# Optimization experiments

Measured on AMD Instinct MI355X. Metric: run time of the kernel, lower is better.

The kernel has to match this reference:

```python
import jax, jax.numpy as jnp
import numpy as np
from jax import lax

SIGMA = 5
RADIUS = int(4 * SIGMA + 0.5)  # 20 -> kernel size 41, pad_size = 41//2 = 20 = RADIUS
D_AP = 2.27
D_DV = 2.27


def _gauss_d1_kernel():
    # gaussian_kernel1d(sigma, order=1, radius): q(x) = -x/sigma^2, kernel = q(x)*phi(x)
    x = np.arange(-RADIUS, RADIUS + 1).astype(np.float64)
    phi = np.exp(-0.5 / SIGMA ** 2 * x ** 2)
    phi = phi / phi.sum()
    return ((-x / SIGMA ** 2) * phi).astype(np.float32)

_KERNEL = jnp.asarray(_gauss_d1_kernel())


def _conv1d_valid(x, k):
    # x: [N, L], k: [K] -> [N, L-K+1]; cross-correlation, same as torch F.conv1d
    return lax.conv_general_dilated(x[:, None, :], k[None, None, :], (1,), 'VALID')[:, 0, :]


def diffY(x):
    # circular padding along H, derivative / dDV
    c, h, w = x.shape
    xp = jnp.pad(x, ((0, 0), (RADIUS, RADIUS), (0, 0)), mode='wrap')
    xp = jnp.transpose(xp, (0, 2, 1)).reshape(c * w, h + 2 * RADIUS)
    out = _conv1d_valid(xp, _KERNEL).reshape(c, w, h)
    return jnp.transpose(out, (0, 2, 1)) / D_DV


def diffX(x):
    # reflect padding along W, derivative / dAP
    c, h, w = x.shape
    xp = jnp.pad(x, ((0, 0), (0, 0), (RADIUS, RADIUS)), mode='reflect')
    out = _conv1d_valid(xp.reshape(c * h, w + 2 * RADIUS), _KERNEL).reshape(c, h, w)
    return out / D_AP


def setup_inputs() -> dict:
    key = jax.random.key(0)
    k1, k2, k3, k4, k5 = jax.random.split(key, 5)
    H, W = 1024, 2048
    return {
        'y': jax.random.normal(k1, (5, H, W), dtype=jnp.float32),
        'v': jax.random.normal(k2, (2, H, W), dtype=jnp.float32),
        'gamma_ds': jax.random.normal(k3, (H, W), dtype=jnp.float32),
        'cad_coefs': jax.random.uniform(k4, (3,), dtype=jnp.float32),
        'myo_coefs': jax.random.uniform(k5, (5,), dtype=jnp.float32),
    }


def reference(y, v, gamma_ds, cad_coefs, myo_coefs):
    H, W = y.shape[-2:]
    m4 = y[:4]                                  # [4,H,W] myosin components
    c1 = y[4:]                                  # [1,H,W] cadherin

    d1_m = jnp.stack([diffY(m4), diffX(m4)], axis=-1).reshape(2, 2, H, W, 2)
    m = m4.reshape(2, 2, H, W)
    d1_c = jnp.stack([diffY(c1), diffX(c1)], axis=-1).reshape(H, W, 2)
    c = c1[0]

    d1_v = jnp.stack([diffY(v), diffX(v)], axis=-1)   # [2,H,W,2]: d1_v[i,y,x,j] = d_j v_i
    gv = jnp.einsum('iyxj->ijyx', d1_v)
    gvT = jnp.einsum('jyxi->ijyx', d1_v)
    O = -0.5 * (gv - gvT)                       # vorticity
    E = 0.5 * (gv + gvT)                        # strain rate

    eye = jnp.eye(2, dtype=y.dtype)[:, :, None, None]
    trm_yx = jnp.einsum('kkyx->yx', m)
    deviatoric = m - 0.5 * trm_yx[None, None] * eye

    m_norm = jnp.sqrt(jnp.sum(m * m, axis=(0, 1), keepdims=True))            # [1,1,H,W]
    m_0 = jnp.mean(m_norm, axis=(2, 3), keepdims=True)                       # [1,1,1,1]
    dev_mag = jnp.sqrt(jnp.sum(deviatoric * deviatoric, axis=(0, 1), keepdims=True))
    devE = jnp.einsum('klyx,klyx->yx', deviatoric, E)[None, None]

    E_active = E - jnp.sign(devE) * devE * deviatoric / dev_mag ** 2
    E_active = 0.5 * E_active * dev_mag / m_0
    E_passive = E - E_active

    mE = (jnp.einsum('ikyx,kjyx->ijyx', m, E_passive)
          + jnp.einsum('ikyx,kjyx->ijyx', E_passive, m))

    cad = jax.nn.relu(cad_coefs)
    myo = jax.nn.relu(myo_coefs)

    cdot = (-jnp.einsum('iyx,yxi->yx', v, d1_c)
            - cad[0] * c
            + cad[1] * c * jnp.einsum('iyxi->yx', d1_v)
            + cad[2] * gamma_ds)

    trm = trm_yx[None, None]
    gamma_dv = jnp.array([[1.0, 0.0], [0.0, 0.0]], dtype=y.dtype)[:, :, None, None]

    mdot = (-jnp.einsum('kyx,ijyxk->ijyx', v, d1_m)
            - jnp.einsum('ikyx,kjyx->ijyx', O, m)
            + jnp.einsum('ikyx,kjyx->ijyx', m, O)
            - myo[0] * m
            + myo[1] * mE
            - myo[2] * c[None, None] * mE
            + myo[3] * trm * gamma_dv
            + myo[4] * trm * m)

    return jnp.concatenate([mdot.reshape(4, H, W), cdot[None]], axis=0)
```

## Files before the change

kernel.cpp:

```cpp
#include <hip/hip_runtime.h>
#include <math.h>

#define RAD 20
#define KLEN 41
#define NH 1024
#define NW 2048
#define NHW (NH * NW)

struct KW { float w[KLEN]; };
constexpr double cexp_neg(double u) {
  double term = 1.0, sum = 1.0;
  for (int k = 1; k < 30; ++k) { term *= (-u) / (double)k; sum += term; }
  return sum;
}
constexpr KW make_kw() {
  KW r{};
  double ph[KLEN] = {};
  double s = 0.0;
  for (int i = 0; i < KLEN; ++i) {
    double d = (double)(i - RAD);
    double e = cexp_neg(d * d / 800.0);
    e = e * e; e = e * e; e = e * e; e = e * e;
    ph[i] = e; s += e;
  }
  for (int i = 0; i < KLEN; ++i) {
    double d = (double)(i - RAD);
    r.w[i] = (float)((-d / 25.0) * (ph[i] / s) / 2.27);
  }
  return r;
}
static constexpr KW KWC = make_kw();

template <int K>
__device__ __forceinline__ void tap(float s, float& r0, float& r1, float& r2,
                                    float& r3, float& r4, float& r5, float& r6,
                                    float& r7) {
  if constexpr (K - 0 >= 0 && K - 0 <= 40) r0 = fmaf(s, KWC.w[K - 0], r0);
  if constexpr (K - 1 >= 0 && K - 1 <= 40) r1 = fmaf(s, KWC.w[K - 1], r1);
  if constexpr (K - 2 >= 0 && K - 2 <= 40) r2 = fmaf(s, KWC.w[K - 2], r2);
  if constexpr (K - 3 >= 0 && K - 3 <= 40) r3 = fmaf(s, KWC.w[K - 3], r3);
  if constexpr (K - 4 >= 0 && K - 4 <= 40) r4 = fmaf(s, KWC.w[K - 4], r4);
  if constexpr (K - 5 >= 0 && K - 5 <= 40) r5 = fmaf(s, KWC.w[K - 5], r5);
  if constexpr (K - 6 >= 0 && K - 6 <= 40) r6 = fmaf(s, KWC.w[K - 6], r6);
  if constexpr (K - 7 >= 0 && K - 7 <= 40) r7 = fmaf(s, KWC.w[K - 7], r7);
}

#define R8 r0, r1, r2, r3, r4, r5, r6, r7

#define TW 64
#define TH 32
#define TILE_CH ((TH + 2 * RAD) * TW)

__device__ __forceinline__ void conv_col(const float* __restrict__ t, int base,
                                         int lane, float& r0, float& r1,
                                         float& r2, float& r3, float& r4,
                                         float& r5, float& r6, float& r7) {
#define CCHUNK(c)                                      \
  {                                                    \
    float s0 = t[(base + 4 * (c) + 0) * TW + lane];    \
    float s1 = t[(base + 4 * (c) + 1) * TW + lane];    \
    float s2 = t[(base + 4 * (c) + 2) * TW + lane];    \
    float s3 = t[(base + 4 * (c) + 3) * TW + lane];    \
    tap<4 * (c) + 0>(s0, R8);                          \
    tap<4 * (c) + 1>(s1, R8);                          \
    tap<4 * (c) + 2>(s2, R8);                          \
    tap<4 * (c) + 3>(s3, R8);                          \
  }
  CCHUNK(0) CCHUNK(1) CCHUNK(2) CCHUNK(3) CCHUNK(4) CCHUNK(5)
  CCHUNK(6) CCHUNK(7) CCHUNK(8) CCHUNK(9) CCHUNK(10) CCHUNK(11)
#undef CCHUNK
}

__global__ __launch_bounds__(256) void k_reduce(const float* __restrict__ y,
                                                double* __restrict__ acc) {
  const int tid = blockIdx.x * blockDim.x + threadIdx.x;
  const int stride = gridDim.x * blockDim.x;
  double local = 0.0;
  for (int q = tid; q < NHW / 4; q += stride) {
    float4 a = ((const float4*)y)[q];
    float4 b = ((const float4*)(y + NHW))[q];
    float4 c = ((const float4*)(y + 2 * (size_t)NHW))[q];
    float4 d = ((const float4*)(y + 3 * (size_t)NHW))[q];
    local += (double)sqrtf(a.x * a.x + b.x * b.x + c.x * c.x + d.x * d.x);
    local += (double)sqrtf(a.y * a.y + b.y * b.y + c.y * c.y + d.y * d.y);
    local += (double)sqrtf(a.z * a.z + b.z * b.z + c.z * c.z + d.z * d.z);
    local += (double)sqrtf(a.w * a.w + b.w * b.w + c.w * c.w + d.w * d.w);
  }
#pragma unroll
  for (int off = 32; off > 0; off >>= 1) local += __shfl_down(local, off, 64);
  __shared__ double smem[4];
  const int lane = threadIdx.x & 63;
  const int wid = threadIdx.x >> 6;
  if (lane == 0) smem[wid] = local;
  __syncthreads();
  if (threadIdx.x == 0) {
    double s = smem[0] + smem[1] + smem[2] + smem[3];
    atomicAdd(acc, s);
  }
}

__global__ __launch_bounds__(256) void k_dx(const float* __restrict__ y,
                                            const float* __restrict__ v,
                                            float* __restrict__ ws) {
  __shared__ float row[2120];
  const int t = threadIdx.x;
  const int r = blockIdx.x;
  const int ch = blockIdx.y;
  const float* src = (ch < 5) ? (y + (size_t)ch * NHW) : (v + (size_t)(ch - 5) * NHW);
  const float* rp = src + (size_t)r * NW;

#define SWZ(i) ((i) + ((i) >> 6))
#define ST(i, val) { const int ii_ = (i); row[SWZ(ii_)] = (val); }

  const float4* rp4 = (const float4*)rp;
  float4 b0 = rp4[t];
  float4 b1 = rp4[t + 256];
  ST(RAD + 4 * t + 0, b0.x)
  ST(RAD + 4 * t + 1, b0.y)
  ST(RAD + 4 * t + 2, b0.z)
  ST(RAD + 4 * t + 3, b0.w)
  ST(RAD + 4 * (t + 256) + 0, b1.x)
  ST(RAD + 4 * (t + 256) + 1, b1.y)
  ST(RAD + 4 * (t + 256) + 2, b1.z)
  ST(RAD + 4 * (t + 256) + 3, b1.w)
  if (t < RAD) {
    ST(t, rp[RAD - t])
    ST(NW + RAD + t, rp[NW - 2 - t])
  }
  __syncthreads();

  const int xb = 8 * t;
  float r0 = 0.f, r1 = 0.f, r2 = 0.f, r3 = 0.f;
  float r4 = 0.f, r5 = 0.f, r6 = 0.f, r7 = 0.f;
#define RD(k) { const int x_ = xb + (k); float s_ = row[SWZ(x_)]; tap<(k)>(s_, R8); }
  RD(0)  RD(1)  RD(2)  RD(3)  RD(4)  RD(5)  RD(6)  RD(7)
  RD(8)  RD(9)  RD(10) RD(11) RD(12) RD(13) RD(14) RD(15)
  RD(16) RD(17) RD(18) RD(19) RD(20) RD(21) RD(22) RD(23)
  RD(24) RD(25) RD(26) RD(27) RD(28) RD(29) RD(30) RD(31)
  RD(32) RD(33) RD(34) RD(35) RD(36) RD(37) RD(38) RD(39)
  RD(40) RD(41) RD(42) RD(43) RD(44) RD(45) RD(46) RD(47)
#undef RD

  float4 o0, o1;
  o0.x = r0; o0.y = r1; o0.z = r2; o0.w = r3;
  o1.x = r4; o1.y = r5; o1.z = r6; o1.w = r7;
  float4* dst = (float4*)(ws + (size_t)(7 + ch) * NHW + (size_t)r * NW + xb);
  dst[0] = o0;
  dst[1] = o1;
}

__global__ __launch_bounds__(256) void k_dyf(
    const float* __restrict__ y, const float* __restrict__ v,
    const float* __restrict__ gds, const float* __restrict__ cadc,
    const float* __restrict__ myoc, const float* __restrict__ ws,
    const double* __restrict__ acc, float* __restrict__ out) {
  __shared__ float tile[4 * TILE_CH];
  const int lane = threadIdx.x & 63;
  const int wid = threadIdx.x >> 6;
  const int x0 = blockIdx.x * TW;
  const int yb = blockIdx.y * TH;
  const int base = wid * 8;

  const float m0 = (float)(acc[0] / (double)NHW);
  const float cad0 = fmaxf(cadc[0], 0.f);
  const float cad1 = fmaxf(cadc[1], 0.f);
  const float cad2 = fmaxf(cadc[2], 0.f);
  const float my0 = fmaxf(myoc[0], 0.f);
  const float my1 = fmaxf(myoc[1], 0.f);
  const float my2 = fmaxf(myoc[2], 0.f);
  const float my3 = fmaxf(myoc[3], 0.f);
  const float my4 = fmaxf(myoc[4], 0.f);

#define SGLD(sp, k) \
  (sp)[(size_t)(((yb - RAD + wid + 4 * (k)) + NH) & (NH - 1)) * NW + x0 + lane]
#define STAGECH(g, srcp)                                                    \
  {                                                                         \
    const float* sp_ = (srcp);                                              \
    float u0 = SGLD(sp_, 0), u1 = SGLD(sp_, 1), u2 = SGLD(sp_, 2);          \
    float u3 = SGLD(sp_, 3), u4 = SGLD(sp_, 4), u5 = SGLD(sp_, 5);          \
    float u6 = SGLD(sp_, 6), u7 = SGLD(sp_, 7), u8 = SGLD(sp_, 8);          \
    float u9 = SGLD(sp_, 9), u10 = SGLD(sp_, 10), u11 = SGLD(sp_, 11);      \
    float u12 = SGLD(sp_, 12), u13 = SGLD(sp_, 13), u14 = SGLD(sp_, 14);    \
    float u15 = SGLD(sp_, 15), u16 = SGLD(sp_, 16), u17 = SGLD(sp_, 17);    \
    float* tb_ = &tile[(g) * TILE_CH];                                      \
    tb_[(wid + 0) * TW + lane] = u0;   tb_[(wid + 4) * TW + lane] = u1;     \
    tb_[(wid + 8) * TW + lane] = u2;   tb_[(wid + 12) * TW + lane] = u3;    \
    tb_[(wid + 16) * TW + lane] = u4;  tb_[(wid + 20) * TW + lane] = u5;    \
    tb_[(wid + 24) * TW + lane] = u6;  tb_[(wid + 28) * TW + lane] = u7;    \
    tb_[(wid + 32) * TW + lane] = u8;  tb_[(wid + 36) * TW + lane] = u9;    \
    tb_[(wid + 40) * TW + lane] = u10; tb_[(wid + 44) * TW + lane] = u11;   \
    tb_[(wid + 48) * TW + lane] = u12; tb_[(wid + 52) * TW + lane] = u13;   \
    tb_[(wid + 56) * TW + lane] = u14; tb_[(wid + 60) * TW + lane] = u15;   \
    tb_[(wid + 64) * TW + lane] = u16; tb_[(wid + 68) * TW + lane] = u17;   \
  }

#define DECL8(P)                                                       \
  float P##0 = 0.f, P##1 = 0.f, P##2 = 0.f, P##3 = 0.f, P##4 = 0.f,    \
        P##5 = 0.f, P##6 = 0.f, P##7 = 0.f;
#define CALLCONV(g, P)                                                  \
  conv_col(&tile[(g) * TILE_CH], base, lane, P##0, P##1, P##2, P##3,    \
           P##4, P##5, P##6, P##7);

  STAGECH(0, y)
  STAGECH(1, y + (size_t)NHW)
  STAGECH(2, y + 2 * (size_t)NHW)
  STAGECH(3, y + 3 * (size_t)NHW)
  __syncthreads();
  DECL8(ym00) DECL8(ym01) DECL8(ym10) DECL8(ym11)
  CALLCONV(0, ym00)
  CALLCONV(1, ym01)
  CALLCONV(2, ym10)
  CALLCONV(3, ym11)
  __syncthreads();

  STAGECH(0, y + 4 * (size_t)NHW)
  STAGECH(1, v)
  STAGECH(2, v + (size_t)NHW)
  __syncthreads();
  DECL8(yc) DECL8(yv0) DECL8(yv1)
  CALLCONV(0, yc)
  CALLCONV(1, yv0)
  CALLCONV(2, yv1)

#define POINT(q)                                                              \
  {                                                                           \
    const size_t idx = (size_t)(yb + base + (q)) * NW + x0 + lane;            \
    const int trow = (RAD + base + (q)) * TW + lane;                          \
    const float m00 = y[idx];                                                 \
    const float m01 = y[idx + (size_t)NHW];                                   \
    const float m10 = y[idx + 2 * (size_t)NHW];                               \
    const float m11 = y[idx + 3 * (size_t)NHW];                               \
    const float c = tile[0 * TILE_CH + trow];                                 \
    const float v0 = tile[1 * TILE_CH + trow];                                \
    const float v1 = tile[2 * TILE_CH + trow];                                \
    const float g = gds[idx];                                                 \
    const float dY_m00 = ym00##q, dY_m01 = ym01##q;                           \
    const float dY_m10 = ym10##q, dY_m11 = ym11##q;                           \
    const float dY_c = yc##q, dY_v0 = yv0##q, dY_v1 = yv1##q;                 \
    const float dX_m00 = ws[idx + 7 * (size_t)NHW];                           \
    const float dX_m01 = ws[idx + 8 * (size_t)NHW];                           \
    const float dX_m10 = ws[idx + 9 * (size_t)NHW];                           \
    const float dX_m11 = ws[idx + 10 * (size_t)NHW];                          \
    const float dX_c = ws[idx + 11 * (size_t)NHW];                            \
    const float dX_v0 = ws[idx + 12 * (size_t)NHW];                           \
    const float dX_v1 = ws[idx + 13 * (size_t)NHW];                           \
    const float gv00 = dY_v0, gv01 = dX_v0, gv10 = dY_v1, gv11 = dX_v1;       \
    const float ww = -0.5f * (gv01 - gv10);                                   \
    const float E00 = gv00, E11 = gv11;                                       \
    const float E01 = 0.5f * (gv01 + gv10);                                   \
    const float E10 = E01;                                                    \
    const float trm = m00 + m11;                                              \
    const float dev00 = m00 - 0.5f * trm;                                     \
    const float dev01 = m01;                                                  \
    const float dev10 = m10;                                                  \
    const float dev11 = m11 - 0.5f * trm;                                     \
    const float dmag_sq =                                                     \
        dev00 * dev00 + dev01 * dev01 + dev10 * dev10 + dev11 * dev11;        \
    const float dm = sqrtf(dmag_sq);                                          \
    const float dm2 = dm * dm;                                                \
    const float devE = dev00 * E00 + dev01 * E01 + dev10 * E10 + dev11 * E11; \
    const float sg = (devE > 0.f) ? 1.f : ((devE < 0.f) ? -1.f : 0.f);        \
    const float coef = sg * devE / dm2;                                       \
    const float sc = 0.5f * dm / m0;                                          \
    const float Ea00 = (E00 - coef * dev00) * sc;                             \
    const float Ea01 = (E01 - coef * dev01) * sc;                             \
    const float Ea10 = (E10 - coef * dev10) * sc;                             \
    const float Ea11 = (E11 - coef * dev11) * sc;                             \
    const float Ep00 = E00 - Ea00;                                            \
    const float Ep01 = E01 - Ea01;                                            \
    const float Ep10 = E10 - Ea10;                                            \
    const float Ep11 = E11 - Ea11;                                            \
    const float mE00 = (m00 * Ep00 + m01 * Ep10) + (Ep00 * m00 + Ep01 * m10); \
    const float mE01 = (m00 * Ep01 + m01 * Ep11) + (Ep00 * m01 + Ep01 * m11); \
    const float mE10 = (m10 * Ep00 + m11 * Ep10) + (Ep10 * m00 + Ep11 * m10); \
    const float mE11 = (m10 * Ep01 + m11 * Ep11) + (Ep10 * m01 + Ep11 * m11); \
    const float divv = gv00 + gv11;                                           \
    const float cdot =                                                        \
        -(v0 * dY_c + v1 * dX_c) - cad0 * c + cad1 * c * divv + cad2 * g;     \
    const float md00 = -(v0 * dY_m00 + v1 * dX_m00) - ww * m10 - ww * m01 -   \
                       my0 * m00 + my1 * mE00 - my2 * c * mE00 + my3 * trm +  \
                       my4 * trm * m00;                                       \
    const float md01 = -(v0 * dY_m01 + v1 * dX_m01) - ww * m11 + ww * m00 -   \
                       my0 * m01 + my1 * mE01 - my2 * c * mE01 +              \
                       my4 * trm * m01;                                       \
    const float md10 = -(v0 * dY_m10 + v1 * dX_m10) + ww * m00 - ww * m11 -   \
                       my0 * m10 + my1 * mE10 - my2 * c * mE10 +              \
                       my4 * trm * m10;                                       \
    const float md11 = -(v0 * dY_m11 + v1 * dX_m11) + ww * m01 + ww * m10 -   \
                       my0 * m11 + my1 * mE11 - my2 * c * mE11 +              \
                       my4 * trm * m11;                                       \
    out[idx] = md00;                                                          \
    out[idx + (size_t)NHW] = md01;                                            \
    out[idx + 2 * (size_t)NHW] = md10;                                        \
    out[idx + 3 * (size_t)NHW] = md11;                                        \
    out[idx + 4 * (size_t)NHW] = cdot;                                        \
  }

  POINT(0) POINT(1) POINT(2) POINT(3)
  POINT(4) POINT(5) POINT(6) POINT(7)
#undef POINT
}

extern "C" void kernel_launch(void* const* d_in, const int* in_sizes, int n_in,
                              void* d_out, int out_size, void* d_ws, size_t ws_size,
                              hipStream_t stream) {
  (void)in_sizes; (void)n_in; (void)out_size; (void)ws_size;
  const float* y = (const float*)d_in[0];
  const float* v = (const float*)d_in[1];
  const float* gds = (const float*)d_in[2];
  const float* cadc = (const float*)d_in[3];
  const float* myoc = (const float*)d_in[4];
  float* out = (float*)d_out;

  double* acc = (double*)d_ws;
  float* planes = (float*)((char*)d_ws + 512);

  hipMemsetAsync(acc, 0, sizeof(double), stream);
  k_reduce<<<dim3(1024), dim3(256), 0, stream>>>(y, acc);
  k_dx<<<dim3(NH, 7), dim3(256), 0, stream>>>(y, v, planes);
  k_dyf<<<dim3(NW / TW, NH / TH), dim3(256), 0, stream>>>(y, v, gds, cadc, myoc,
                                                          planes, acc, out);
}
```

Before: 179.7 us.

## Double-buffer LDS channel staging to overlap global loads with convolution

Replaces the four-channel and three-channel LDS staging with a two-slot ping-pong buffer. Each channel's global loads are issued into registers before the convolution on the previous slot runs, then written to the other slot. This halves shared memory per block and adds an occupancy hint of 4 blocks per SM through launch bounds. In exchange it uses more barriers, and c, v0 and v1 are now re-read from global memory instead of LDS.

```diff
diff --git a/kernel.cpp b/kernel.cpp
--- a/kernel.cpp
+++ b/kernel.cpp
@@ -149,12 +149,12 @@
   dst[1] = o1;
 }
 
-__global__ __launch_bounds__(256) void k_dyf(
+__global__ __launch_bounds__(256, 4) void k_dyf(
     const float* __restrict__ y, const float* __restrict__ v,
     const float* __restrict__ gds, const float* __restrict__ cadc,
     const float* __restrict__ myoc, const float* __restrict__ ws,
     const double* __restrict__ acc, float* __restrict__ out) {
-  __shared__ float tile[4 * TILE_CH];
+  __shared__ float tile[2 * TILE_CH];
   const int lane = threadIdx.x & 63;
   const int wid = threadIdx.x >> 6;
   const int x0 = blockIdx.x * TW;
@@ -173,27 +173,33 @@
 
 #define SGLD(sp, k) \
   (sp)[(size_t)(((yb - RAD + wid + 4 * (k)) + NH) & (NH - 1)) * NW + x0 + lane]
-#define STAGECH(g, srcp)                                                    \
-  {                                                                         \
-    const float* sp_ = (srcp);                                              \
-    float u0 = SGLD(sp_, 0), u1 = SGLD(sp_, 1), u2 = SGLD(sp_, 2);          \
-    float u3 = SGLD(sp_, 3), u4 = SGLD(sp_, 4), u5 = SGLD(sp_, 5);          \
-    float u6 = SGLD(sp_, 6), u7 = SGLD(sp_, 7), u8 = SGLD(sp_, 8);          \
-    float u9 = SGLD(sp_, 9), u10 = SGLD(sp_, 10), u11 = SGLD(sp_, 11);      \
-    float u12 = SGLD(sp_, 12), u13 = SGLD(sp_, 13), u14 = SGLD(sp_, 14);    \
-    float u15 = SGLD(sp_, 15), u16 = SGLD(sp_, 16), u17 = SGLD(sp_, 17);    \
-    float* tb_ = &tile[(g) * TILE_CH];                                      \
-    tb_[(wid + 0) * TW + lane] = u0;   tb_[(wid + 4) * TW + lane] = u1;     \
-    tb_[(wid + 8) * TW + lane] = u2;   tb_[(wid + 12) * TW + lane] = u3;    \
-    tb_[(wid + 16) * TW + lane] = u4;  tb_[(wid + 20) * TW + lane] = u5;    \
-    tb_[(wid + 24) * TW + lane] = u6;  tb_[(wid + 28) * TW + lane] = u7;    \
-    tb_[(wid + 32) * TW + lane] = u8;  tb_[(wid + 36) * TW + lane] = u9;    \
-    tb_[(wid + 40) * TW + lane] = u10; tb_[(wid + 44) * TW + lane] = u11;   \
-    tb_[(wid + 48) * TW + lane] = u12; tb_[(wid + 52) * TW + lane] = u13;   \
-    tb_[(wid + 56) * TW + lane] = u14; tb_[(wid + 60) * TW + lane] = u15;   \
-    tb_[(wid + 64) * TW + lane] = u16; tb_[(wid + 68) * TW + lane] = u17;   \
-  }
-
+
+  float u0, u1, u2, u3, u4, u5, u6, u7, u8;
+  float u9, u10, u11, u12, u13, u14, u15, u16, u17;
+
+#define LOADCH(srcp)                                                   \
+  {                                                                    \
+    const float* sp_ = (srcp);                                         \
+    u0 = SGLD(sp_, 0); u1 = SGLD(sp_, 1); u2 = SGLD(sp_, 2);           \
+    u3 = SGLD(sp_, 3); u4 = SGLD(sp_, 4); u5 = SGLD(sp_, 5);           \
+    u6 = SGLD(sp_, 6); u7 = SGLD(sp_, 7); u8 = SGLD(sp_, 8);           \
+    u9 = SGLD(sp_, 9); u10 = SGLD(sp_, 10); u11 = SGLD(sp_, 11);       \
+    u12 = SGLD(sp_, 12); u13 = SGLD(sp_, 13); u14 = SGLD(sp_, 14);     \
+    u15 = SGLD(sp_, 15); u16 = SGLD(sp_, 16); u17 = SGLD(sp_, 17);     \
+  }
+#define WRITECH(g)                                                        \
+  {                                                                       \
+    float* tb_ = &tile[(g) * TILE_CH];                                    \
+    tb_[(wid + 0) * TW + lane] = u0;   tb_[(wid + 4) * TW + lane] = u1;   \
+    tb_[(wid + 8) * TW + lane] = u2;   tb_[(wid + 12) * TW + lane] = u3;  \
+    tb_[(wid + 16) * TW + lane] = u4;  tb_[(wid + 20) * TW + lane] = u5;  \
+    tb_[(wid + 24) * TW + lane] = u6;  tb_[(wid + 28) * TW + lane] = u7;  \
+    tb_[(wid + 32) * TW + lane] = u8;  tb_[(wid + 36) * TW + lane] = u9;  \
+    tb_[(wid + 40) * TW + lane] = u10; tb_[(wid + 44) * TW + lane] = u11; \
+    tb_[(wid + 48) * TW + lane] = u12; tb_[(wid + 52) * TW + lane] = u13; \
+    tb_[(wid + 56) * TW + lane] = u14; tb_[(wid + 60) * TW + lane] = u15; \
+    tb_[(wid + 64) * TW + lane] = u16; tb_[(wid + 68) * TW + lane] = u17; \
+  }
 #define DECL8(P)                                                       \
   float P##0 = 0.f, P##1 = 0.f, P##2 = 0.f, P##3 = 0.f, P##4 = 0.f,    \
         P##5 = 0.f, P##6 = 0.f, P##7 = 0.f;
@@ -201,38 +207,48 @@
   conv_col(&tile[(g) * TILE_CH], base, lane, P##0, P##1, P##2, P##3,    \
            P##4, P##5, P##6, P##7);
 
-  STAGECH(0, y)
-  STAGECH(1, y + (size_t)NHW)
-  STAGECH(2, y + 2 * (size_t)NHW)
-  STAGECH(3, y + 3 * (size_t)NHW)
-  __syncthreads();
   DECL8(ym00) DECL8(ym01) DECL8(ym10) DECL8(ym11)
+  DECL8(yc) DECL8(yv0) DECL8(yv1)
+
+  LOADCH(y)
+  WRITECH(0)
+  __syncthreads();
+  LOADCH(y + (size_t)NHW)
   CALLCONV(0, ym00)
+  WRITECH(1)
+  __syncthreads();
+  LOADCH(y + 2 * (size_t)NHW)
   CALLCONV(1, ym01)
-  CALLCONV(2, ym10)
-  CALLCONV(3, ym11)
-  __syncthreads();
-
-  STAGECH(0, y + 4 * (size_t)NHW)
-  STAGECH(1, v)
-  STAGECH(2, v + (size_t)NHW)
-  __syncthreads();
-  DECL8(yc) DECL8(yv0) DECL8(yv1)
+  WRITECH(0)
+  __syncthreads();
+  LOADCH(y + 3 * (size_t)NHW)
+  CALLCONV(0, ym10)
+  WRITECH(1)
+  __syncthreads();
+  LOADCH(y + 4 * (size_t)NHW)
+  CALLCONV(1, ym11)
+  WRITECH(0)
+  __syncthreads();
+  LOADCH(v)
   CALLCONV(0, yc)
+  WRITECH(1)
+  __syncthreads();
+  LOADCH(v + (size_t)NHW)
   CALLCONV(1, yv0)
-  CALLCONV(2, yv1)
+  WRITECH(0)
+  __syncthreads();
+  CALLCONV(0, yv1)
 
 #define POINT(q)                                                              \
   {                                                                           \
     const size_t idx = (size_t)(yb + base + (q)) * NW + x0 + lane;            \
-    const int trow = (RAD + base + (q)) * TW + lane;                          \
     const float m00 = y[idx];                                                 \
     const float m01 = y[idx + (size_t)NHW];                                   \
     const float m10 = y[idx + 2 * (size_t)NHW];                               \
     const float m11 = y[idx + 3 * (size_t)NHW];                               \
-    const float c = tile[0 * TILE_CH + trow];                                 \
-    const float v0 = tile[1 * TILE_CH + trow];                                \
-    const float v1 = tile[2 * TILE_CH + trow];                                \
+    const float c = y[idx + 4 * (size_t)NHW];                                 \
+    const float v0 = v[idx];                                                  \
+    const float v1 = v[idx + (size_t)NHW];                                    \
     const float g = gds[idx];                                                 \
     const float dY_m00 = ym00##q, dY_m01 = ym01##q;                           \
     const float dY_m10 = ym10##q, dY_m11 = ym11##q;                           \
```

New measurement: 179.6 us. No clear change (-0.1%).
